# Kernel optimization log

Hardware: AMD Instinct MI355X
Metric: run time of the kernel (lower is better)

The kernel has to match this reference:

```python
import jax, jax.numpy as jnp
import numpy as np
from jax import lax

WS = 8       # window size
NH = 16      # num heads
ATT = 64     # att_dim
CH_SCALE = ((ATT // NH) // 2) ** (-0.5)  # (head_dim // key_channels_reduction)**-0.5


def dwconv3(x, w, b):
    # depthwise 3x3, SAME padding; w: [C,1,3,3]
    y = lax.conv_general_dilated(x, w, (1, 1), 'SAME',
                                 feature_group_count=x.shape[1],
                                 dimension_numbers=('NCHW', 'OIHW', 'NCHW'))
    return y + b[None, :, None, None]


def conv1x1(x, w, b):
    # w: [O, C]
    return jnp.einsum('bchw,oc->bohw', x, w) + b[None, :, None, None]


def bn(x, g, b, m, v, eps=1e-5):
    s = g / jnp.sqrt(v + eps)
    return (x - m[None, :, None, None]) * s[None, :, None, None] + b[None, :, None, None]


def to_win(t, h, ws):
    # [B, h*d, H, W] -> [(B*hh*ww), h, ws*ws, d]
    B, C, H, W = t.shape
    d, hh, ww = C // h, H // ws, W // ws
    t = t.reshape(B, h, d, hh, ws, ww, ws).transpose(0, 3, 5, 1, 4, 6, 2)
    return t.reshape(B * hh * ww, h, ws * ws, d)


def from_win(t, B, h, ws, hh, ww):
    # [(B*hh*ww), h, ws*ws, d] -> [B, h*d, H, W]
    d = t.shape[-1]
    t = t.reshape(B, hh, ww, h, ws, ws, d).transpose(0, 3, 6, 1, 4, 2, 5)
    return t.reshape(B, h * d, hh * ws, ww * ws)


def setup_inputs() -> dict:
    key = jax.random.key(0)
    ks = jax.random.split(key, 16)
    C, ATTD, QKC, HID = 64, 64, 32, 256
    B, H, W = 2, 512, 512
    inp = {
        'x': jax.random.normal(ks[0], (B, C, H, W), jnp.float32),
        'pa_w': jax.random.normal(ks[1], (C, 1, 3, 3), jnp.float32) * 0.1,
        'pa_b': jnp.zeros((C,), jnp.float32),
        'bn1_g': jnp.ones((ATTD,), jnp.float32), 'bn1_b': jnp.zeros((ATTD,), jnp.float32),
        'bn1_m': jnp.zeros((ATTD,), jnp.float32), 'bn1_v': jnp.ones((ATTD,), jnp.float32),
        'q_w': jax.random.normal(ks[2], (QKC, C), jnp.float32) * 0.05,
        'q_b': jnp.zeros((QKC,), jnp.float32),
        'k_w': jax.random.normal(ks[3], (QKC, C), jnp.float32) * 0.05,
        'k_b': jnp.zeros((QKC,), jnp.float32),
        'v_w': jax.random.normal(ks[4], (ATTD, C), jnp.float32) * 0.05,
        'v_b': jnp.zeros((ATTD,), jnp.float32),
        'hp_w': jax.random.normal(ks[5], (ATTD, ATTD), jnp.float32) * 0.05,
        'hp_b': jnp.zeros((ATTD,), jnp.float32),
        'bn2_g': jnp.ones((ATTD,), jnp.float32), 'bn2_b': jnp.zeros((ATTD,), jnp.float32),
        'bn2_m': jnp.zeros((ATTD,), jnp.float32), 'bn2_v': jnp.ones((ATTD,), jnp.float32),
        'fc1_w': jax.random.normal(ks[6], (HID, ATTD), jnp.float32) * 0.05,
        'fc1_b': jnp.zeros((HID,), jnp.float32),
        'dw_w': jax.random.normal(ks[7], (HID, 1, 3, 3), jnp.float32) * 0.1,
        'dw_b': jnp.zeros((HID,), jnp.float32),
        'bn3_g': jnp.ones((HID,), jnp.float32), 'bn3_b': jnp.zeros((HID,), jnp.float32),
        'bn3_m': jnp.zeros((HID,), jnp.float32), 'bn3_v': jnp.ones((HID,), jnp.float32),
        'fc2_w': jax.random.normal(ks[8], (ATTD, HID), jnp.float32) * 0.05,
        'fc2_b': jnp.zeros((ATTD,), jnp.float32),
    }
    return inp


def reference(x, pa_w, pa_b, bn1_g, bn1_b, bn1_m, bn1_v, q_w, q_b, k_w, k_b,
              v_w, v_b, hp_w, hp_b, bn2_g, bn2_b, bn2_m, bn2_v, fc1_w, fc1_b,
              dw_w, dw_b, bn3_g, bn3_b, bn3_m, bn3_v, fc2_w, fc2_b):
    B, C, H, W = x.shape
    # H, W are multiples of WS, so the reflect pad is a no-op.
    # PA positional attention
    x = x * jax.nn.sigmoid(dwconv3(x, pa_w, pa_b))
    shortcut = x  # [:, :, :H, :W] is identity here
    xn = bn(x, bn1_g, bn1_b, bn1_m, bn1_v)
    q = conv1x1(xn, q_w, q_b)
    k = conv1x1(xn, k_w, k_b)
    v = conv1x1(xn, v_w, v_b)
    hh, ww = H // WS, W // WS
    q = to_win(q, NH, WS)   # [Bw, h, n, dk]
    k = to_win(k, NH, WS)   # [Bw, h, n, dk]
    v = to_win(v, NH, WS)   # [Bw, h, n, dv]
    q = jax.nn.softmax(q, axis=-1)
    k = jax.nn.softmax(k, axis=-2)
    ctx = jnp.einsum('whnd,whne->whde', k, v)          # [Bw, h, dk, dv]
    attn = jnp.einsum('whnd,whde->whne', q, ctx)        # [Bw, h, n, dv]
    dots = jnp.swapaxes(jnp.einsum('whnd,whne->whde', q, k), -2, -1) * CH_SCALE
    dc = (jnp.max(dots, axis=(-2, -1), keepdims=True) +
          jnp.mean(dots, axis=(-2, -1), keepdims=True))  # [Bw, h, 1, 1]
    attn = attn * dc
    s1 = from_win(attn, B, NH, WS, hh, ww)              # [B, ATT, H, W]
    s1 = conv1x1(s1, hp_w, hp_b) + shortcut
    # MLP block
    s2 = bn(s1, bn2_g, bn2_b, bn2_m, bn2_v)
    s2 = conv1x1(s2, fc1_w, fc1_b)
    s2 = jax.nn.gelu(s2, approximate=False)
    s2 = bn(dwconv3(s2, dw_w, dw_b), bn3_g, bn3_b, bn3_m, bn3_v)
    s2 = conv1x1(s2, fc2_w, fc2_b)
    return s1 + s2
```

## Files before the change

kernel.cpp:

```cpp
#include <hip/hip_runtime.h>
#include <stdint.h>

#define HH 512
#define WW 512
#define HW 262144
#define CH 64
#define HID 256

typedef __attribute__((ext_vector_type(8))) short short8;
typedef __attribute__((ext_vector_type(4))) float f32x4;
typedef _Float16 f16x2 __attribute__((ext_vector_type(2)));
typedef _Float16 f16x8 __attribute__((ext_vector_type(8)));

#define WS_QKVB 0
#define WS_F1B  128
#define WS_F2B  384
#define WS_DWP  448
#define WS_W1F  1600
#define WS_W2F  9792
#define WS_WQKV 17984
#define WS_WHP  22080

__device__ __forceinline__ float bf2f(uint16_t u) {
    return __uint_as_float(((uint32_t)u) << 16);
}
__device__ __forceinline__ uint16_t f2bf(float f) {
    uint32_t x = __float_as_uint(f);
    uint32_t r = x + 0x7fffu + ((x >> 16) & 1u);
    return (uint16_t)(r >> 16);
}
__device__ __forceinline__ float h2f(uint16_t u) {
    _Float16 h;
    __builtin_memcpy(&h, &u, 2);
    return (float)h;
}
__device__ __forceinline__ uint16_t f2h(float f) {
    _Float16 h = (_Float16)f;
    uint16_t u;
    __builtin_memcpy(&u, &h, 2);
    return u;
}
__device__ __forceinline__ f16x2 u2h2(uint32_t u) {
    f16x2 r;
    __builtin_memcpy(&r, &u, 4);
    return r;
}
__device__ __forceinline__ uint32_t pkrtz_u32(float a, float b) {
    auto v = __builtin_amdgcn_cvt_pkrtz(a, b);
    uint32_t u;
    __builtin_memcpy(&u, &v, 4);
    return u;
}

__device__ __forceinline__ float gelu_f(float v) {
    float v2 = v * v;
    float m  = v * (-1.5957691216f - 0.0713548162726f * v2);
    float e  = __expf(m);
    return v * __builtin_amdgcn_rcpf(1.f + e);
}

__global__ __launch_bounds__(256) void k0_fold(
    const float* __restrict__ q_w, const float* __restrict__ q_b,
    const float* __restrict__ k_w, const float* __restrict__ k_b,
    const float* __restrict__ v_w, const float* __restrict__ v_b,
    const float* __restrict__ bn1_g, const float* __restrict__ bn1_b,
    const float* __restrict__ bn1_m, const float* __restrict__ bn1_v,
    const float* __restrict__ fc1_w, const float* __restrict__ fc1_b,
    const float* __restrict__ bn2_g, const float* __restrict__ bn2_b,
    const float* __restrict__ bn2_m, const float* __restrict__ bn2_v,
    const float* __restrict__ fc2_w, const float* __restrict__ fc2_b,
    const float* __restrict__ hp_w,
    const float* __restrict__ dw_w, const float* __restrict__ dw_b,
    const float* __restrict__ bn3_g, const float* __restrict__ bn3_b,
    const float* __restrict__ bn3_m, const float* __restrict__ bn3_v,
    float* __restrict__ wsw)
{
    __shared__ float s1s[64], t1s[64], s2s[64], t2s[64], s3s[256], t3s[256];
    int tid = threadIdx.x;
    if (tid < 64) {
        float s = bn1_g[tid] * rsqrtf(bn1_v[tid] + 1e-5f);
        s1s[tid] = s; t1s[tid] = bn1_b[tid] - bn1_m[tid] * s;
        float s2 = bn2_g[tid] * rsqrtf(bn2_v[tid] + 1e-5f);
        s2s[tid] = s2; t2s[tid] = bn2_b[tid] - bn2_m[tid] * s2;
    }
    if (tid < 256) {
        float s = bn3_g[tid] * rsqrtf(bn3_v[tid] + 1e-5f);
        s3s[tid] = s;
        t3s[tid] = (dw_b[tid] - bn3_m[tid]) * s + bn3_b[tid];
    }
    __syncthreads();

    float* qkvb = wsw + WS_QKVB;
    float* f1b  = wsw + WS_F1B;
    float* f2b  = wsw + WS_F2B;
    uint16_t* dwph  = (uint16_t*)(wsw + WS_DWP);
    uint16_t* w1f   = (uint16_t*)(wsw + WS_W1F);
    uint16_t* w2f   = (uint16_t*)(wsw + WS_W2F);
    uint16_t* wqkvf = (uint16_t*)(wsw + WS_WQKV);
    uint16_t* whpf  = (uint16_t*)(wsw + WS_WHP);

    if (tid < 128) {
        int o = tid;
        float a;
        if (o < 32) {
            a = q_b[o];
            for (int c = 0; c < 64; c++) a += q_w[o*64+c]*t1s[c];
        } else if (o < 64) {
            a = k_b[o-32];
            for (int c = 0; c < 64; c++) a += k_w[(o-32)*64+c]*t1s[c];
        } else {
            a = v_b[o-64];
            for (int c = 0; c < 64; c++) a += v_w[(o-64)*64+c]*t1s[c];
        }
        qkvb[o] = a;
    }
    if (tid < 256) {
        float a = fc1_b[tid];
        for (int c = 0; c < 64; c++) a += fc1_w[tid*64+c]*t2s[c];
        f1b[tid] = a;
    }
    if (tid < 64) {
        float a = fc2_b[tid];
        for (int c = 0; c < 256; c++) a += fc2_w[tid*256+c]*t3s[c];
        f2b[tid] = a;
    }
    for (int i = tid; i < 8192; i += 256) {
        int nt = i >> 10, rem = i & 1023;
        int k8 = rem >> 7, col = (rem >> 3) & 15, j = rem & 7;
        int o = nt*16 + col, c = k8*8 + j;
        float w;
        if (o < 32)      w = q_w[o*64 + c];
        else if (o < 64) w = k_w[(o-32)*64 + c];
        else             w = v_w[(o-64)*64 + c];
        wqkvf[i] = f2bf(w * s1s[c]);
    }
    for (int i = tid; i < 4096; i += 256) {
        int mt = i >> 10, rem = i & 1023;
        int k8 = rem >> 7, row = (rem >> 3) & 15, j = rem & 7;
        int o = mt*16 + row, c = k8*8 + j;
        whpf[i] = f2bf(hp_w[o*64 + c]);
    }
    for (int i = tid; i < 16384; i += 256) {
        int nt = i >> 10, rem = i & 1023;
        int k8 = rem >> 7, col = (rem >> 3) & 15, j = rem & 7;
        int c = k8*8 + j, o = nt*16 + col;
        w1f[i] = f2bf(fc1_w[o*64 + c] * s2s[c]);
    }
    for (int i = tid; i < 16384; i += 256) {
        int nt = i >> 12, rem = i & 4095;
        int k8 = rem >> 7, col = (rem >> 3) & 15, j = rem & 7;
        int c = k8*8 + j, o = nt*16 + col;
        w2f[i] = f2h(fc2_w[o*256 + c] * s3s[c]);
    }
    for (int i = tid; i < 2304; i += 256) {
        int t = i >> 8, ch = i & 255;
        dwph[i] = f2h(dw_w[ch*9 + t]);
    }
}

__global__ __launch_bounds__(256, 4) void k2_attn(
    const float* __restrict__ x,
    const float* __restrict__ pa_w, const float* __restrict__ pa_b,
    const float* __restrict__ hp_b,
    const float* __restrict__ wsw, uint16_t* __restrict__ s1out)
{
    __shared__ __align__(16) uint16_t qkv[8704];
    __shared__ __align__(16) uint16_t gfrag[4096];
    __shared__ __align__(16) uint16_t afrag[4096];

    int tid = threadIdx.x;
    int wave = tid >> 6, l = tid & 63;
    int orig = blockIdx.x;
    int wid = (orig & 7) * 1024 + (orig >> 3);
    int b = wid >> 12;
    int r = wid & 4095;
    int wy = r >> 6, wx = r & 63;
    int y0 = wy*8 - 1;
    const float* xb = x + (size_t)b * CH * HW;

    {
        int c = tid & 63, yh = tid >> 6;
        float pw[9];
        #pragma unroll
        for (int t = 0; t < 9; t++) pw[t] = pa_w[c*9 + t];
        float pb = pa_b[c];
        const float* xc = xb + (size_t)c * HW;
        int px0 = wx*8 - 2;

        float va[4][12];
        #pragma unroll
        for (int tr = 0; tr < 4; tr++) {
            int yy = y0 + yh*2 + tr;
            if ((unsigned)yy < 512u) {
                const float* rp = xc + (size_t)yy*512 + px0;
                float2 s0 = {0.f, 0.f}, s3 = {0.f, 0.f};
                if (wx > 0)  s0 = *reinterpret_cast<const float2*>(rp);
                float4 s1v = *reinterpret_cast<const float4*>(rp + 2);
                float4 s2v = *reinterpret_cast<const float4*>(rp + 6);
                if (wx < 63) s3 = *reinterpret_cast<const float2*>(rp + 10);
                va[tr][0]=s0.x;  va[tr][1]=s0.y;
                va[tr][2]=s1v.x; va[tr][3]=s1v.y; va[tr][4]=s1v.z; va[tr][5]=s1v.w;
                va[tr][6]=s2v.x; va[tr][7]=s2v.y; va[tr][8]=s2v.z; va[tr][9]=s2v.w;
                va[tr][10]=s3.x; va[tr][11]=s3.y;
            } else {
                #pragma unroll
                for (int s = 0; s < 12; s++) va[tr][s] = 0.f;
            }
        }
        #pragma unroll
        for (int dy2 = 0; dy2 < 2; dy2++) {
            int y = yh*2 + dy2;
            #pragma unroll
            for (int xx = 0; xx < 8; xx++) {
                float conv = pb;
                #pragma unroll
                for (int dy = 0; dy < 3; dy++)
                    #pragma unroll
                    for (int dx = 0; dx < 3; dx++)
                        conv += va[dy2+dy][xx+1+dx] * pw[dy*3+dx];
                float xcv = va[dy2+1][xx+2];
                float gv = xcv / (1.f + __expf(-conv));
                int n = y*8 + xx;
                gfrag[(n>>4)*1024 + (c>>3)*128 + (n&15)*8 + (c&7)] = f2bf(gv);
            }
        }
    }
    __syncthreads();

    {
        const uint16_t* wqkv = (const uint16_t*)(wsw + WS_WQKV);
        const float* qkvb = wsw + WS_QKVB;
        f32x4 acc[4][2];
        #pragma unroll
        for (int ntw = 0; ntw < 2; ntw++) {
            float bias = qkvb[(wave*2+ntw)*16 + (l & 15)];
            #pragma unroll
            for (int mt = 0; mt < 4; mt++) acc[mt][ntw] = {bias, bias, bias, bias};
        }
        #pragma unroll
        for (int kb = 0; kb < 2; kb++) {
            short8 a[4];
            #pragma unroll
            for (int mt = 0; mt < 4; mt++)
                a[mt] = *reinterpret_cast<const short8*>(&gfrag[mt*1024 + kb*512 + 8*l]);
            #pragma unroll
            for (int ntw = 0; ntw < 2; ntw++) {
                int nt = wave*2 + ntw;
                short8 bf = *reinterpret_cast<const short8*>(&wqkv[nt*1024 + kb*512 + 8*l]);
                #pragma unroll
                for (int mt = 0; mt < 4; mt++)
                    acc[mt][ntw] = __builtin_amdgcn_mfma_f32_16x16x32_bf16(a[mt], bf, acc[mt][ntw], 0, 0, 0);
            }
        }
        #pragma unroll
        for (int ntw = 0; ntw < 2; ntw++) {
            int o = (wave*2+ntw)*16 + (l & 15);
            #pragma unroll
            for (int mt = 0; mt < 4; mt++) {
                int px0 = mt*16 + (l >> 4)*4;
                uint32_t lo = pkrtz_u32(acc[mt][ntw][0], acc[mt][ntw][1]);
                uint32_t hi = pkrtz_u32(acc[mt][ntw][2], acc[mt][ntw][3]);
                *reinterpret_cast<uint64_t*>(&qkv[o*68 + px0]) =
                    (uint64_t)lo | ((uint64_t)hi << 32);
            }
        }
    }
    __syncthreads();

    {
        int hd = tid >> 4, l16 = tid & 15;
        float a0[4], a1[4], a2[4], a3[4], a4[4], a5[4], a6[4], a7[4];
        #pragma unroll
        for (int j = 0; j < 4; j++) {
            int px = l16 + 16*j;
            a0[j] = h2f(qkv[(2*hd    )*68 + px]);
            a1[j] = h2f(qkv[(2*hd + 1)*68 + px]);
            a2[j] = h2f(qkv[(32 + 2*hd    )*68 + px]);
            a3[j] = h2f(qkv[(32 + 2*hd + 1)*68 + px]);
            a4[j] = h2f(qkv[(64 + 4*hd    )*68 + px]);
            a5[j] = h2f(qkv[(64 + 4*hd + 1)*68 + px]);
            a6[j] = h2f(qkv[(64 + 4*hd + 2)*68 + px]);
            a7[j] = h2f(qkv[(64 + 4*hd + 3)*68 + px]);
        }
        #pragma unroll
        for (int j = 0; j < 4; j++) {
            float m = fmaxf(a0[j], a1[j]);
            float e0 = __expf(a0[j]-m), e1 = __expf(a1[j]-m);
            float inv = 1.f/(e0+e1);
            a0[j] = e0*inv; a1[j] = e1*inv;
        }
        float m0 = fmaxf(fmaxf(a2[0],a2[1]), fmaxf(a2[2],a2[3]));
        float m1 = fmaxf(fmaxf(a3[0],a3[1]), fmaxf(a3[2],a3[3]));
        #pragma unroll
        for (int s = 1; s < 16; s <<= 1) {
            m0 = fmaxf(m0, __shfl_xor(m0, s, 64));
            m1 = fmaxf(m1, __shfl_xor(m1, s, 64));
        }
        float sum0 = 0.f, sum1 = 0.f;
        #pragma unroll
        for (int j = 0; j < 4; j++) {
            a2[j] = __expf(a2[j]-m0); a3[j] = __expf(a3[j]-m1);
            sum0 += a2[j]; sum1 += a3[j];
        }
        #pragma unroll
        for (int s = 1; s < 16; s <<= 1) {
            sum0 += __shfl_xor(sum0, s, 64);
            sum1 += __shfl_xor(sum1, s, 64);
        }
        float iv0 = 1.f/sum0, iv1 = 1.f/sum1;
        #pragma unroll
        for (int j = 0; j < 4; j++) { a2[j] *= iv0; a3[j] *= iv1; }
        float ctx0[4], ctx1[4];
        #pragma unroll
        for (int e = 0; e < 4; e++) {
            float ve0, ve1, ve2, ve3;
            if (e==0) { ve0=a4[0]; ve1=a4[1]; ve2=a4[2]; ve3=a4[3]; }
            else if (e==1) { ve0=a5[0]; ve1=a5[1]; ve2=a5[2]; ve3=a5[3]; }
            else if (e==2) { ve0=a6[0]; ve1=a6[1]; ve2=a6[2]; ve3=a6[3]; }
            else { ve0=a7[0]; ve1=a7[1]; ve2=a7[2]; ve3=a7[3]; }
            float c0 = a2[0]*ve0 + a2[1]*ve1 + a2[2]*ve2 + a2[3]*ve3;
            float c1 = a3[0]*ve0 + a3[1]*ve1 + a3[2]*ve2 + a3[3]*ve3;
            #pragma unroll
            for (int s = 1; s < 16; s <<= 1) {
                c0 += __shfl_xor(c0, s, 64);
                c1 += __shfl_xor(c1, s, 64);
            }
            ctx0[e] = c0; ctx1[e] = c1;
        }
        float p00=0.f, p01=0.f, p10=0.f, p11=0.f;
        #pragma unroll
        for (int j = 0; j < 4; j++) {
            p00 += a0[j]*a2[j]; p01 += a0[j]*a3[j];
            p10 += a1[j]*a2[j]; p11 += a1[j]*a3[j];
        }
        #pragma unroll
        for (int s = 1; s < 16; s <<= 1) {
            p00 += __shfl_xor(p00, s, 64); p01 += __shfl_xor(p01, s, 64);
            p10 += __shfl_xor(p10, s, 64); p11 += __shfl_xor(p11, s, 64);
        }
        const float CH_SCALE = 0.70710678118654752f;
        p00 *= CH_SCALE; p01 *= CH_SCALE; p10 *= CH_SCALE; p11 *= CH_SCALE;
        float dc = fmaxf(fmaxf(p00,p01), fmaxf(p10,p11)) + 0.25f*(p00+p01+p10+p11);

        #pragma unroll
        for (int j = 0; j < 4; j++) {
            uint16_t t[4];
            #pragma unroll
            for (int e = 0; e < 4; e++)
                t[e] = f2bf((a0[j]*ctx0[e] + a1[j]*ctx1[e]) * dc);
            *reinterpret_cast<uint64_t*>(
                &afrag[j*1024 + (hd>>1)*128 + l16*8 + (hd&1)*4]) =
                *reinterpret_cast<const uint64_t*>(t);
        }
    }
    __syncthreads();

    {
        const uint16_t* whp = (const uint16_t*)(wsw + WS_WHP);
        int nt = wave;
        f32x4 oacc[4];
        #pragma unroll
        for (int mt = 0; mt < 4; mt++) {
            int o0 = mt*16 + (l >> 4)*4;
            float4 hb = *reinterpret_cast<const float4*>(&hp_b[o0]);
            oacc[mt] = {hb.x, hb.y, hb.z, hb.w};
        }
        #pragma unroll
        for (int kb = 0; kb < 2; kb++) {
            short8 bf = *reinterpret_cast<const short8*>(&afrag[nt*1024 + kb*512 + 8*l]);
            #pragma unroll
            for (int mt = 0; mt < 4; mt++) {
                short8 a = *reinterpret_cast<const short8*>(&whp[mt*1024 + kb*512 + 8*l]);
                oacc[mt] = __builtin_amdgcn_mfma_f32_16x16x32_bf16(a, bf, oacc[mt], 0, 0, 0);
            }
        }
        int px = nt*16 + (l & 15);
        int yy = wy*8 + (px >> 3), xx = wx*8 + (px & 7);
        size_t pbase = ((size_t)b * HW + (size_t)yy * 512 + xx) * 64;
        #pragma unroll
        for (int mt = 0; mt < 4; mt++) {
            int o0 = mt*16 + (l >> 4)*4;
            uint64_t gg = *reinterpret_cast<const uint64_t*>(
                &gfrag[(px>>4)*1024 + (o0>>3)*128 + (px&15)*8 + (o0&7)]);
            uint16_t t[4];
            #pragma unroll
            for (int rr = 0; rr < 4; rr++) {
                float g = bf2f((uint16_t)(gg >> (16*rr)));
                t[rr] = f2bf(oacc[mt][rr] + g);
            }
            *reinterpret_cast<uint64_t*>(&s1out[pbase + o0]) =
                *reinterpret_cast<const uint64_t*>(t);
        }
    }
}

__global__ __launch_bounds__(256, 4) void k3_mlp(
    const uint16_t* __restrict__ s1b, const float* __restrict__ wsw,
    float* __restrict__ out)
{
    __shared__ __align__(16) uint16_t sfrag[12288];
    __shared__ __align__(16) uint16_t hbuf[6480];

    const float* f1b = wsw + WS_F1B;
    const float* f2b = wsw + WS_F2B;
    const uint16_t* dwph = (const uint16_t*)(wsw + WS_DWP);
    const uint16_t* w1f  = (const uint16_t*)(wsw + WS_W1F);
    const uint16_t* w2f  = (const uint16_t*)(wsw + WS_W2F);

    int tid = threadIdx.x;
    int wave = tid >> 6, l = tid & 63;
    int hxl = l & 15, cg = l >> 4;
    int X0 = blockIdx.x * 16, Y0 = blockIdx.y * 8;
    int b = blockIdx.z;

    for (int i = tid; i < 1440; i += 256) {
        int px = i >> 3, g = i & 7;
        int hy = px / 18, hx = px - hy*18;
        int yy = Y0 - 1 + hy, xx = X0 - 1 + hx;
        uint4 q = {0u, 0u, 0u, 0u};
        if ((unsigned)yy < 512u && (unsigned)xx < 512u)
            q = *reinterpret_cast<const uint4*>(
                &s1b[((size_t)b*HW + (size_t)yy*512 + xx)*64 + g*8]);
        *reinterpret_cast<uint4*>(&sfrag[(px>>4)*1024 + g*128 + (px&15)*8]) = q;
    }

    f32x4 acc[2][4];
    #pragma unroll
    for (int nt = 0; nt < 4; nt++) {
        float bias = f2b[nt*16 + (l & 15)];
        acc[0][nt] = {bias, bias, bias, bias};
        acc[1][nt] = acc[0][nt];
    }
    __syncthreads();

    for (int cc = 0; cc < 8; cc++) {
        short8 wA[2][2];
        #pragma unroll
        for (int mtw = 0; mtw < 2; mtw++)
            #pragma unroll
            for (int kb = 0; kb < 2; kb++)
                wA[mtw][kb] = *reinterpret_cast<const short8*>(
                    &w1f[(cc*2 + mtw)*1024 + kb*512 + 8*l]);
        float4 hb0 = *reinterpret_cast<const float4*>(&f1b[cc*32      + cg*4]);
        float4 hb1 = *reinterpret_cast<const float4*>(&f1b[cc*32 + 16 + cg*4]);

        for (int pt = wave; pt < 12; pt += 4) {
            f32x4 h0 = {hb0.x, hb0.y, hb0.z, hb0.w};
            f32x4 h1 = {hb1.x, hb1.y, hb1.z, hb1.w};
            #pragma unroll
            for (int kb = 0; kb < 2; kb++) {
                short8 bf = *reinterpret_cast<const short8*>(&sfrag[pt*1024 + kb*512 + 8*l]);
                h0 = __builtin_amdgcn_mfma_f32_16x16x32_bf16(wA[0][kb], bf, h0, 0, 0, 0);
                h1 = __builtin_amdgcn_mfma_f32_16x16x32_bf16(wA[1][kb], bf, h1, 0, 0, 0);
            }
            int px = pt*16 + hxl;
            if (px < 180) {
                int hy = px / 18, hx = px - hy*18;
                bool img = ((unsigned)(Y0-1+hy) < 512u) && ((unsigned)(X0-1+hx) < 512u);
                uint64_t v0 = 0, v1 = 0;
                if (img) {
                    uint32_t a01 = pkrtz_u32(gelu_f(h0[0]), gelu_f(h0[1]));
                    uint32_t a23 = pkrtz_u32(gelu_f(h0[2]), gelu_f(h0[3]));
                    uint32_t b01 = pkrtz_u32(gelu_f(h1[0]), gelu_f(h1[1]));
                    uint32_t b23 = pkrtz_u32(gelu_f(h1[2]), gelu_f(h1[3]));
                    v0 = (uint64_t)a01 | ((uint64_t)a23 << 32);
                    v1 = (uint64_t)b01 | ((uint64_t)b23 << 32);
                }
                int base = px*36 + cg*4;
                *reinterpret_cast<uint64_t*>(&hbuf[base])      = v0;
                *reinterpret_cast<uint64_t*>(&hbuf[base + 16]) = v1;
            }
        }
        __syncthreads();

        f16x8 bfr[4];
        #pragma unroll
        for (int nt = 0; nt < 4; nt++)
            bfr[nt] = *reinterpret_cast<const f16x8*>(&w2f[nt*4096 + cc*512 + 8*l]);

        uint4 R[4][3];
        #pragma unroll
        for (int tr = 0; tr < 4; tr++)
            #pragma unroll
            for (int dx = 0; dx < 3; dx++)
                R[tr][dx] = *reinterpret_cast<const uint4*>(
                    &hbuf[((wave*2 + tr)*18 + hxl + dx)*36 + cg*8]);

        union { f16x2 h[4]; f16x8 v; } t0, t1;
        f16x2 z = {(_Float16)0.f, (_Float16)0.f};
        #pragma unroll
        for (int g = 0; g < 4; g++) { t0.h[g] = z; t1.h[g] = z; }

        #pragma unroll
        for (int dy = 0; dy < 3; dy++) {
            #pragma unroll
            for (int dx = 0; dx < 3; dx++) {
                uint4 w = *reinterpret_cast<const uint4*>(
                    &dwph[(dy*3+dx)*256 + cc*32 + cg*8]);
                uint4 qa = R[dy][dx];
                uint4 qb = R[dy+1][dx];
                t0.h[0] += u2h2(qa.x) * u2h2(w.x);
                t0.h[1] += u2h2(qa.y) * u2h2(w.y);
                t0.h[2] += u2h2(qa.z) * u2h2(w.z);
                t0.h[3] += u2h2(qa.w) * u2h2(w.w);
                t1.h[0] += u2h2(qb.x) * u2h2(w.x);
                t1.h[1] += u2h2(qb.y) * u2h2(w.y);
                t1.h[2] += u2h2(qb.z) * u2h2(w.z);
                t1.h[3] += u2h2(qb.w) * u2h2(w.w);
            }
        }
        #pragma unroll
        for (int nt = 0; nt < 4; nt++) {
            acc[0][nt] = __builtin_amdgcn_mfma_f32_16x16x32_f16(t0.v, bfr[nt], acc[0][nt], 0, 0, 0);
            acc[1][nt] = __builtin_amdgcn_mfma_f32_16x16x32_f16(t1.v, bfr[nt], acc[1][nt], 0, 0, 0);
        }
        __syncthreads();
    }

    int r0 = cg * 4;
    #pragma unroll
    for (int mi = 0; mi < 2; mi++) {
        int yrow = Y0 + wave*2 + mi;
        size_t srow = ((size_t)b*HW + (size_t)yrow*512 + X0 + r0) * 64;
        #pragma unroll
        for (int nt = 0; nt < 4; nt++) {
            int o = nt*16 + (l & 15);
            size_t oidx = ((size_t)b*CH + o)*HW + (size_t)yrow*512 + X0 + r0;
            float4 ov;
            ov.x = acc[mi][nt][0] + bf2f(s1b[srow + o]);
            ov.y = acc[mi][nt][1] + bf2f(s1b[srow + 64 + o]);
            ov.z = acc[mi][nt][2] + bf2f(s1b[srow + 128 + o]);
            ov.w = acc[mi][nt][3] + bf2f(s1b[srow + 192 + o]);
            *reinterpret_cast<float4*>(out + oidx) = ov;
        }
    }
}

extern "C" void kernel_launch(void* const* d_in, const int* in_sizes, int n_in,
                              void* d_out, int out_size, void* d_ws, size_t ws_size,
                              hipStream_t stream) {
    const float* x     = (const float*)d_in[0];
    const float* pa_w  = (const float*)d_in[1];
    const float* pa_b  = (const float*)d_in[2];
    const float* bn1_g = (const float*)d_in[3];
    const float* bn1_b = (const float*)d_in[4];
    const float* bn1_m = (const float*)d_in[5];
    const float* bn1_v = (const float*)d_in[6];
    const float* q_w   = (const float*)d_in[7];
    const float* q_b   = (const float*)d_in[8];
    const float* k_w   = (const float*)d_in[9];
    const float* k_b   = (const float*)d_in[10];
    const float* v_w   = (const float*)d_in[11];
    const float* v_b   = (const float*)d_in[12];
    const float* hp_w  = (const float*)d_in[13];
    const float* hp_b  = (const float*)d_in[14];
    const float* bn2_g = (const float*)d_in[15];
    const float* bn2_b = (const float*)d_in[16];
    const float* bn2_m = (const float*)d_in[17];
    const float* bn2_v = (const float*)d_in[18];
    const float* fc1_w = (const float*)d_in[19];
    const float* fc1_b = (const float*)d_in[20];
    const float* dw_w  = (const float*)d_in[21];
    const float* dw_b  = (const float*)d_in[22];
    const float* bn3_g = (const float*)d_in[23];
    const float* bn3_b = (const float*)d_in[24];
    const float* bn3_m = (const float*)d_in[25];
    const float* bn3_v = (const float*)d_in[26];
    const float* fc2_w = (const float*)d_in[27];
    const float* fc2_b = (const float*)d_in[28];

    uint16_t* s1b = (uint16_t*)d_ws;
    float*    wsw = (float*)((char*)d_ws + 134217728 + 268435456);

    k0_fold<<<dim3(1), dim3(256), 0, stream>>>(
        q_w, q_b, k_w, k_b, v_w, v_b,
        bn1_g, bn1_b, bn1_m, bn1_v,
        fc1_w, fc1_b, bn2_g, bn2_b, bn2_m, bn2_v,
        fc2_w, fc2_b, hp_w, dw_w, dw_b, bn3_g, bn3_b, bn3_m, bn3_v, wsw);

    k2_attn<<<dim3(8192), dim3(256), 0, stream>>>(
        x, pa_w, pa_b, hp_b, wsw, s1b);

    k3_mlp<<<dim3(32, 64, 2), dim3(256), 0, stream>>>(
        s1b, wsw, (float*)d_out);
}
```

Measured before the change: 342.4 us.

## Stage x tile in shared bf16 for attention conv; hoist MLP index math

In the attention kernel, the 10x16 halo tile of x for all 64 channels is now loaded cooperatively with coalesced float4 reads, converted to bf16, and stored in shared memory that aliases the qkv buffer. The depthwise gate conv then reads from shared memory instead of issuing per-thread strided global loads. In the MLP kernel, interior blocks skip bounds checks when loading the halo, and the per-tile pixel index, mask and hbuf offset are precomputed once outside the channel loop. This trades a larger shared buffer, an extra barrier and bf16 rounding of the conv input for fewer and better-coalesced global loads and less repeated integer math.

Result: faster. 292.7 us (-14.5%).

```diff
diff --git a/kernel.cpp b/kernel.cpp
--- a/kernel.cpp
+++ b/kernel.cpp
@@ -164,9 +164,11 @@
     const float* __restrict__ hp_b,
     const float* __restrict__ wsw, uint16_t* __restrict__ s1out)
 {
-    __shared__ __align__(16) uint16_t qkv[8704];
+    __shared__ __align__(16) uint16_t regionA[10880];
     __shared__ __align__(16) uint16_t gfrag[4096];
     __shared__ __align__(16) uint16_t afrag[4096];
+    uint16_t* xs  = regionA;
+    uint16_t* qkv = regionA;
 
     int tid = threadIdx.x;
     int wave = tid >> 6, l = tid & 63;
@@ -176,7 +178,45 @@
     int r = wid & 4095;
     int wy = r >> 6, wx = r & 63;
     int y0 = wy*8 - 1;
+    int x0g = wx*8 - 4;
     const float* xb = x + (size_t)b * CH * HW;
+    bool interior = (wy > 0) & (wy < 63) & (wx > 0) & (wx < 63);
+
+    if (interior) {
+        #pragma unroll
+        for (int k = 0; k < 10; k++) {
+            int i = k*256 + tid;
+            int seg = i & 3;
+            int rem = i >> 2;
+            int c = rem / 10;
+            int py = rem - c*10;
+            const float* src = xb + (size_t)c*HW + (size_t)(y0+py)*512 + x0g + seg*4;
+            float4 v = *reinterpret_cast<const float4*>(src);
+            uint16_t tv[4] = {f2bf(v.x), f2bf(v.y), f2bf(v.z), f2bf(v.w)};
+            *reinterpret_cast<uint64_t*>(&xs[c*170 + py*16 + seg*4]) =
+                *reinterpret_cast<const uint64_t*>(tv);
+        }
+    } else {
+        #pragma unroll
+        for (int k = 0; k < 10; k++) {
+            int i = k*256 + tid;
+            int seg = i & 3;
+            int rem = i >> 2;
+            int c = rem / 10;
+            int py = rem - c*10;
+            int yy = y0 + py;
+            int gx = x0g + seg*4;
+            uint64_t v64 = 0;
+            if ((unsigned)yy < 512u && (unsigned)gx <= 508u) {
+                float4 v = *reinterpret_cast<const float4*>(
+                    xb + (size_t)c*HW + (size_t)yy*512 + gx);
+                uint16_t tv[4] = {f2bf(v.x), f2bf(v.y), f2bf(v.z), f2bf(v.w)};
+                v64 = *reinterpret_cast<const uint64_t*>(tv);
+            }
+            *reinterpret_cast<uint64_t*>(&xs[c*170 + py*16 + seg*4]) = v64;
+        }
+    }
+    __syncthreads();
 
     {
         int c = tid & 63, yh = tid >> 6;
@@ -184,27 +224,15 @@
         #pragma unroll
         for (int t = 0; t < 9; t++) pw[t] = pa_w[c*9 + t];
         float pb = pa_b[c];
-        const float* xc = xb + (size_t)c * HW;
-        int px0 = wx*8 - 2;
-
         float va[4][12];
         #pragma unroll
         for (int tr = 0; tr < 4; tr++) {
-            int yy = y0 + yh*2 + tr;
-            if ((unsigned)yy < 512u) {
-                const float* rp = xc + (size_t)yy*512 + px0;
-                float2 s0 = {0.f, 0.f}, s3 = {0.f, 0.f};
-                if (wx > 0)  s0 = *reinterpret_cast<const float2*>(rp);
-                float4 s1v = *reinterpret_cast<const float4*>(rp + 2);
-                float4 s2v = *reinterpret_cast<const float4*>(rp + 6);
-                if (wx < 63) s3 = *reinterpret_cast<const float2*>(rp + 10);
-                va[tr][0]=s0.x;  va[tr][1]=s0.y;
-                va[tr][2]=s1v.x; va[tr][3]=s1v.y; va[tr][4]=s1v.z; va[tr][5]=s1v.w;
-                va[tr][6]=s2v.x; va[tr][7]=s2v.y; va[tr][8]=s2v.z; va[tr][9]=s2v.w;
-                va[tr][10]=s3.x; va[tr][11]=s3.y;
-            } else {
-                #pragma unroll
-                for (int s = 0; s < 12; s++) va[tr][s] = 0.f;
+            const uint16_t* rp = &xs[c*170 + (yh*2 + tr)*16];
+            #pragma unroll
+            for (int s = 0; s < 6; s++) {
+                uint32_t u = *reinterpret_cast<const uint32_t*>(&rp[2 + s*2]);
+                va[tr][s*2]   = __uint_as_float(u << 16);
+                va[tr][s*2+1] = __uint_as_float(u & 0xffff0000u);
             }
         }
         #pragma unroll
@@ -412,16 +440,42 @@
     int hxl = l & 15, cg = l >> 4;
     int X0 = blockIdx.x * 16, Y0 = blockIdx.y * 8;
     int b = blockIdx.z;
-
-    for (int i = tid; i < 1440; i += 256) {
-        int px = i >> 3, g = i & 7;
+    bool interior = (X0 > 0) & (X0 < 496) & (Y0 > 0) & (Y0 < 504);
+
+    if (interior) {
+        for (int i = tid; i < 1440; i += 256) {
+            int px = i >> 3, g = i & 7;
+            int hy = px / 18, hx = px - hy*18;
+            int yy = Y0 - 1 + hy, xx = X0 - 1 + hx;
+            uint4 q = *reinterpret_cast<const uint4*>(
+                &s1b[((size_t)b*HW + (size_t)yy*512 + xx)*64 + g*8]);
+            *reinterpret_cast<uint4*>(&sfrag[(px>>4)*1024 + g*128 + (px&15)*8]) = q;
+        }
+    } else {
+        for (int i = tid; i < 1440; i += 256) {
+            int px = i >> 3, g = i & 7;
+            int hy = px / 18, hx = px - hy*18;
+            int yy = Y0 - 1 + hy, xx = X0 - 1 + hx;
+            uint4 q = {0u, 0u, 0u, 0u};
+            if ((unsigned)yy < 512u && (unsigned)xx < 512u)
+                q = *reinterpret_cast<const uint4*>(
+                    &s1b[((size_t)b*HW + (size_t)yy*512 + xx)*64 + g*8]);
+            *reinterpret_cast<uint4*>(&sfrag[(px>>4)*1024 + g*128 + (px&15)*8]) = q;
+        }
+    }
+
+    bool okA[3], imgA[3];
+    int hbA[3], ptA[3];
+    #pragma unroll
+    for (int it = 0; it < 3; it++) {
+        int pt = wave + it*4;
+        int px = pt*16 + hxl;
+        ptA[it] = pt;
+        okA[it] = px < 180;
         int hy = px / 18, hx = px - hy*18;
-        int yy = Y0 - 1 + hy, xx = X0 - 1 + hx;
-        uint4 q = {0u, 0u, 0u, 0u};
-        if ((unsigned)yy < 512u && (unsigned)xx < 512u)
-            q = *reinterpret_cast<const uint4*>(
-                &s1b[((size_t)b*HW + (size_t)yy*512 + xx)*64 + g*8]);
-        *reinterpret_cast<uint4*>(&sfrag[(px>>4)*1024 + g*128 + (px&15)*8]) = q;
+        imgA[it] = okA[it] &&
+            (interior || (((unsigned)(Y0-1+hy) < 512u) && ((unsigned)(X0-1+hx) < 512u)));
+        hbA[it] = px*36 + cg*4;
     }
 
     f32x4 acc[2][4];
@@ -444,7 +498,9 @@
         float4 hb0 = *reinterpret_cast<const float4*>(&f1b[cc*32      + cg*4]);
         float4 hb1 = *reinterpret_cast<const float4*>(&f1b[cc*32 + 16 + cg*4]);
 
-        for (int pt = wave; pt < 12; pt += 4) {
+        #pragma unroll
+        for (int it = 0; it < 3; it++) {
+            int pt = ptA[it];
             f32x4 h0 = {hb0.x, hb0.y, hb0.z, hb0.w};
             f32x4 h1 = {hb1.x, hb1.y, hb1.z, hb1.w};
             #pragma unroll
@@ -453,12 +509,9 @@
                 h0 = __builtin_amdgcn_mfma_f32_16x16x32_bf16(wA[0][kb], bf, h0, 0, 0, 0);
                 h1 = __builtin_amdgcn_mfma_f32_16x16x32_bf16(wA[1][kb], bf, h1, 0, 0, 0);
             }
-            int px = pt*16 + hxl;
-            if (px < 180) {
-                int hy = px / 18, hx = px - hy*18;
-                bool img = ((unsigned)(Y0-1+hy) < 512u) && ((unsigned)(X0-1+hx) < 512u);
+            if (okA[it]) {
                 uint64_t v0 = 0, v1 = 0;
-                if (img) {
+                if (imgA[it]) {
                     uint32_t a01 = pkrtz_u32(gelu_f(h0[0]), gelu_f(h0[1]));
                     uint32_t a23 = pkrtz_u32(gelu_f(h0[2]), gelu_f(h0[3]));
                     uint32_t b01 = pkrtz_u32(gelu_f(h1[0]), gelu_f(h1[1]));
@@ -466,9 +519,8 @@
                     v0 = (uint64_t)a01 | ((uint64_t)a23 << 32);
                     v1 = (uint64_t)b01 | ((uint64_t)b23 << 32);
                 }
-                int base = px*36 + cg*4;
-                *reinterpret_cast<uint64_t*>(&hbuf[base])      = v0;
-                *reinterpret_cast<uint64_t*>(&hbuf[base + 16]) = v1;
+                *reinterpret_cast<uint64_t*>(&hbuf[hbA[it]])      = v0;
+                *reinterpret_cast<uint64_t*>(&hbuf[hbA[it] + 16]) = v1;
             }
         }
         __syncthreads();
```
